# Performance work log

Measured on AMD Instinct MI355X. Metric: run time of the kernel, lower is better.

## Reference

```python
import jax, jax.numpy as jnp
import numpy as np

N = 100000   # nodes
E = 1600000  # edges
IN = 92      # input node feature dim
H = 128      # hidden dim
B = 512      # graphs in batch
GI = 107     # global_info feature dim
L = 5        # conv layers
EPS = 1e-5   # batchnorm eps


def setup_inputs() -> dict:
    key = jax.random.key(0)
    ks = jax.random.split(key, 32)
    s = 0.05
    rn = lambda k, shp: jax.random.normal(k, shp, jnp.float32) * s
    return {
        "x": jax.random.normal(ks[0], (N, IN), jnp.float32),
        "edge_index": jax.random.randint(ks[1], (2, E), 0, N, jnp.int32),
        "edge_dist": jax.random.uniform(ks[2], (E,), jnp.float32),
        "global_info": jax.random.normal(ks[3], (N, GI), jnp.float32),
        "batch": jnp.sort(jax.random.randint(ks[4], (N,), 0, B, jnp.int32)),
        # input projection
        "lin_W": rn(ks[5], (IN, H)), "lin_b": rn(ks[6], (H,)),
        # GCN conv stack
        "conv_W": rn(ks[7], (L, H, H)), "conv_b": rn(ks[8], (L, H)),
        # shared batchnorm affine
        "bn_g": jnp.ones((H,), jnp.float32), "bn_b": jnp.zeros((H,), jnp.float32),
        # global attention
        "gat_in_W": rn(ks[9], (H + GI, H)), "gat_in_b": rn(ks[10], (H,)),
        "gat_lin_W": rn(ks[11], (2, H, H)), "gat_lin_b": rn(ks[12], (2, H)),
        "gat_out_W": rn(ks[13], (H, 1)), "gat_out_b": rn(ks[14], (1,)),
        # Set2Set LSTM (input 2H, hidden H)
        "lstm_Wih": rn(ks[15], (4 * H, 2 * H)), "lstm_Whh": rn(ks[16], (4 * H, H)),
        "lstm_bih": rn(ks[17], (4 * H,)), "lstm_bhh": rn(ks[18], (4 * H,)),
        # MLP head (in_dim = 2H)
        "mlp_W": rn(ks[19], (2 * H, 2 * H)), "mlp_b": rn(ks[20], (2 * H,)),
        "out1_W": rn(ks[21], (2 * H, 32)), "out1_b": rn(ks[22], (32,)),
        "out2_W": rn(ks[23], (32, 1)), "out2_b": rn(ks[24], (1,)),
    }


def _segment_softmax(e, seg, num_seg):
    m = jax.ops.segment_max(e, seg, num_seg)
    ex = jnp.exp(e - m[seg])
    return ex / jax.ops.segment_sum(ex, seg, num_seg)[seg]


def reference(x, edge_index, edge_dist, global_info, batch,
              lin_W, lin_b, conv_W, conv_b, bn_g, bn_b,
              gat_in_W, gat_in_b, gat_lin_W, gat_lin_b, gat_out_W, gat_out_b,
              lstm_Wih, lstm_Whh, lstm_bih, lstm_bhh,
              mlp_W, mlp_b, out1_W, out1_b, out2_W, out2_b):
    src, dst = edge_index[0], edge_index[1]

    x = jax.nn.relu(x @ lin_W + lin_b)

    # GCN normalization (improved=True: self-loop weight 2), identical each layer
    deg = jax.ops.segment_sum(edge_dist, dst, N) + 2.0
    dinv = jax.lax.rsqrt(deg)
    enorm = dinv[src] * edge_dist * dinv[dst]   # [E]
    self_norm = 2.0 * dinv * dinv               # [N]

    prev = x
    for l in range(L):
        xw = x @ conv_W[l]                                                  # [N,H]
        agg = (jax.ops.segment_sum(enorm[:, None] * xw[src], dst, N)
               + self_norm[:, None] * xw + conv_b[l])
        mu = agg.mean(0)
        var = agg.var(0)
        h = bn_g * (agg - mu) * jax.lax.rsqrt(var + EPS) + bn_b             # BN (batch stats)
        x = h + prev                                                         # residual; dropout=identity (eval)
        prev = x

    # global attention -> per-graph softmax node weights
    g = jax.nn.relu(jnp.concatenate([x, global_info], axis=-1) @ gat_in_W + gat_in_b)
    for l in range(2):
        g = jax.nn.relu(g @ gat_lin_W[l] + gat_lin_b[l])
    e = (g @ gat_out_W + gat_out_b)[:, 0]                                    # [N]
    w = _segment_softmax(e, batch, B)
    x = x * w[:, None]

    # Set2Set pooling, 3 processing steps
    hs = jnp.zeros((B, H), x.dtype)
    cs = jnp.zeros((B, H), x.dtype)
    q_star = jnp.zeros((B, 2 * H), x.dtype)
    for _ in range(3):
        gates = q_star @ lstm_Wih.T + hs @ lstm_Whh.T + lstm_bih + lstm_bhh
        i, f, gg, o = jnp.split(gates, 4, axis=-1)
        cs = jax.nn.sigmoid(f) * cs + jax.nn.sigmoid(i) * jnp.tanh(gg)
        hs = jax.nn.sigmoid(o) * jnp.tanh(cs)
        q = hs                                                                # [B,H]
        en = jnp.sum(x * q[batch], axis=-1)                                   # [N]
        a = _segment_softmax(en, batch, B)
        r = jax.ops.segment_sum(a[:, None] * x, batch, B)                      # [B,H]
        q_star = jnp.concatenate([q, r], axis=-1)

    # MLP head
    y = jax.nn.relu(q_star @ mlp_W + mlp_b)
    y = jax.nn.relu(y @ out1_W + out1_b)
    y = y @ out2_W + out2_b
    return y.reshape(1, -1)
```

## Files before the change

kernel.cpp:

```cpp
#include <hip/hip_runtime.h>
#include <math.h>

#define NN 100000
#define NE 1600000
#define DIN 92
#define H 128
#define NB 512
#define DGI 107
#define NL 5

typedef unsigned short u16;
typedef unsigned long long u64;
typedef short bf16x8 __attribute__((ext_vector_type(8)));
typedef float f32x4 __attribute__((ext_vector_type(4)));
typedef _Float16 f16;
typedef _Float16 f16x8 __attribute__((ext_vector_type(8)));
typedef unsigned short u16x8 __attribute__((ext_vector_type(8)));

__device__ __forceinline__ u16 f2bf(float f) {
    unsigned u = __builtin_bit_cast(unsigned, f);
    u += 0x7FFF + ((u >> 16) & 1);
    return (u16)(u >> 16);
}
__device__ __forceinline__ float bf2f(u16 h) {
    unsigned u = ((unsigned)h) << 16;
    return __builtin_bit_cast(float, u);
}

__global__ void __launch_bounds__(128) k_split(const float* __restrict__ src, int Ksrc, int ld_src,
                                               u16* __restrict__ hi, u16* __restrict__ lo,
                                               int ld_dst, int col_off, int Kfill)
{
    int row = blockIdx.x;
    int k = blockIdx.y * 128 + threadIdx.x;
    if (k >= Kfill) return;
    float v = (k < Ksrc) ? src[(size_t)row * ld_src + k] : 0.f;
    u16 h = f2bf(v);
    float r = v - bf2f(h);
    size_t o = (size_t)row * ld_dst + col_off + k;
    hi[o] = h;
    lo[o] = f2bf(r);
}

struct WJobs {
    const float* W[9];
    long long eoff[9];
    int K[9];
    int Kpad[9];
};

__global__ void __launch_bounds__(128) k_splitW_all(WJobs jobs, u16* __restrict__ wthi, u16* __restrict__ wtlo)
{
    int j = blockIdx.z;
    int c = blockIdx.x;
    int k = blockIdx.y * 128 + threadIdx.x;
    int Kp = jobs.Kpad[j];
    if (k >= Kp) return;
    const float* W = jobs.W[j];
    float v = (k < jobs.K[j]) ? W[(size_t)k * H + c] : 0.f;
    u16 h = f2bf(v);
    float r = v - bf2f(h);
    size_t o = (size_t)jobs.eoff[j] + (size_t)c * Kp + k;
    wthi[o] = h;
    wtlo[o] = f2bf(r);
}

#define GBM 128

template<int RELU, int OMODE>
__global__ void __launch_bounds__(256) k_mgemm(
    const u16* __restrict__ A1hi, const u16* __restrict__ A1lo, int lda1, int K1,
    const u16* __restrict__ A2hi, const u16* __restrict__ A2lo, int lda2,
    const u16* __restrict__ Wthi, const u16* __restrict__ Wtlo, int Kpad,
    const float* __restrict__ bias,
    float* __restrict__ Cf, u16* __restrict__ Chi, u16* __restrict__ Clo, int ldsp,
    f16* __restrict__ Ch,
    const float* __restrict__ Gow, const float* __restrict__ GobP, float* __restrict__ Esc,
    int M)
{
    __shared__ __align__(16) u16 As[2][128][40];
    __shared__ __align__(16) u16 Ws[2][128][40];
    int tid = threadIdx.x;
    int w = tid >> 6, l = tid & 63;
    int row0 = blockIdx.x * GBM;
    int lr = l & 15, kq = l >> 4;

    f32x4 acc[2][8];
#pragma unroll
    for (int rf = 0; rf < 2; ++rf)
#pragma unroll
        for (int cf = 0; cf < 8; ++cf)
            acc[rf][cf] = (f32x4){0.f, 0.f, 0.f, 0.f};

    for (int k0 = 0; k0 < Kpad; k0 += 32) {
        const u16* sAh = (k0 < K1) ? A1hi : A2hi;
        const u16* sAl = (k0 < K1) ? A1lo : A2lo;
        int ldc = (k0 < K1) ? lda1 : lda2;
        int kc = (k0 < K1) ? k0 : (k0 - K1);
#pragma unroll
        for (int i = 0; i < 2; ++i) {
            int chunk = tid + i * 256;
            int r = chunk >> 2, q = chunk & 3;
            int gr = row0 + r; if (gr >= M) gr = M - 1;
            int4 va = *(const int4*)(sAh + (size_t)gr * ldc + kc + q * 8);
            int4 vb = *(const int4*)(sAl + (size_t)gr * ldc + kc + q * 8);
            int4 wa = *(const int4*)(Wthi + (size_t)r * Kpad + k0 + q * 8);
            int4 wb = *(const int4*)(Wtlo + (size_t)r * Kpad + k0 + q * 8);
            *(int4*)&As[0][r][q * 8] = va;
            *(int4*)&As[1][r][q * 8] = vb;
            *(int4*)&Ws[0][r][q * 8] = wa;
            *(int4*)&Ws[1][r][q * 8] = wb;
        }
        __syncthreads();

        bf16x8 aH[2], aL[2];
#pragma unroll
        for (int rf = 0; rf < 2; ++rf) {
            aH[rf] = *(const bf16x8*)&As[0][w * 32 + rf * 16 + lr][kq * 8];
            aL[rf] = *(const bf16x8*)&As[1][w * 32 + rf * 16 + lr][kq * 8];
        }
#pragma unroll
        for (int cf = 0; cf < 8; ++cf) {
            bf16x8 bH = *(const bf16x8*)&Ws[0][cf * 16 + lr][kq * 8];
            bf16x8 bL = *(const bf16x8*)&Ws[1][cf * 16 + lr][kq * 8];
#pragma unroll
            for (int rf = 0; rf < 2; ++rf) {
                acc[rf][cf] = __builtin_amdgcn_mfma_f32_16x16x32_bf16(aH[rf], bH, acc[rf][cf], 0, 0, 0);
                acc[rf][cf] = __builtin_amdgcn_mfma_f32_16x16x32_bf16(aH[rf], bL, acc[rf][cf], 0, 0, 0);
                acc[rf][cf] = __builtin_amdgcn_mfma_f32_16x16x32_bf16(aL[rf], bH, acc[rf][cf], 0, 0, 0);
            }
        }
        __syncthreads();
    }

    if (OMODE == 3) {
        float gowv[8], bvv[8];
#pragma unroll
        for (int cf = 0; cf < 8; ++cf) {
            gowv[cf] = Gow[cf * 16 + lr];
            bvv[cf] = bias[cf * 16 + lr];
        }
        float gob0 = GobP[0];
#pragma unroll
        for (int rf = 0; rf < 2; ++rf) {
#pragma unroll
            for (int r = 0; r < 4; ++r) {
                float part = 0.f;
#pragma unroll
                for (int cf = 0; cf < 8; ++cf) {
                    float v = fmaxf(acc[rf][cf][r] + bvv[cf], 0.f);
                    part += v * gowv[cf];
                }
                part += __shfl_xor(part, 1);
                part += __shfl_xor(part, 2);
                part += __shfl_xor(part, 4);
                part += __shfl_xor(part, 8);
                int grow = row0 + w * 32 + rf * 16 + kq * 4 + r;
                if (lr == 0 && grow < M) Esc[grow] = part + gob0;
            }
        }
        return;
    }

#pragma unroll
    for (int cf = 0; cf < 8; ++cf) {
        int col = cf * 16 + lr;
        float bv = bias ? bias[col] : 0.f;
#pragma unroll
        for (int rf = 0; rf < 2; ++rf) {
#pragma unroll
            for (int r = 0; r < 4; ++r) {
                int grow = row0 + w * 32 + rf * 16 + kq * 4 + r;
                if (grow < M) {
                    float v = acc[rf][cf][r] + bv;
                    if (RELU) v = fmaxf(v, 0.f);
                    if (OMODE == 0) Cf[(size_t)grow * H + col] = v;
                    if (OMODE == 1) {
                        u16 hh = f2bf(v);
                        Chi[(size_t)grow * ldsp + col] = hh;
                        Clo[(size_t)grow * ldsp + col] = f2bf(v - bf2f(hh));
                    }
                    if (OMODE == 2) Ch[(size_t)grow * H + col] = (f16)v;
                }
            }
        }
    }
}

__global__ void __launch_bounds__(256) k_deg2(const int* __restrict__ dst, const float* __restrict__ ed,
                                              u64* __restrict__ degcnt, int* __restrict__ rank)
{
    int e = blockIdx.x * 256 + threadIdx.x;
    if (e < NE) {
        int d = dst[e];
        u64 pk = ((u64)1 << 40) | (u64)(ed[e] * 16777216.0f);
        u64 old = atomicAdd(&degcnt[d], pk);
        rank[e] = (int)(old >> 40);
    }
}

__global__ void __launch_bounds__(256) k_dinv2(const u64* __restrict__ degcnt,
                                               float* __restrict__ dinv, float* __restrict__ selfn,
                                               int* __restrict__ cnt)
{
    int n = blockIdx.x * 256 + threadIdx.x;
    if (n < NN) {
        u64 v = degcnt[n];
        int c = (int)(v >> 40);
        float deg = (float)((double)(v & (((u64)1 << 40) - 1)) * (1.0 / 16777216.0));
        float d = deg + 2.0f;
        float dv = 1.0f / sqrtf(d);
        dinv[n] = dv;
        selfn[n] = 2.0f * dv * dv;
        cnt[n] = c;
    }
}

__global__ void __launch_bounds__(256) k_blocksum(const int* __restrict__ cnt, int* __restrict__ bsum, int n)
{
    __shared__ int red[256];
    int t = threadIdx.x;
    int base = blockIdx.x * 1024;
    int s = 0;
#pragma unroll
    for (int j = 0; j < 4; ++j) {
        int i = base + j * 256 + t;
        if (i < n) s += cnt[i];
    }
    red[t] = s; __syncthreads();
    for (int off = 128; off; off >>= 1) {
        if (t < off) red[t] += red[t + off];
        __syncthreads();
    }
    if (t == 0) bsum[blockIdx.x] = red[0];
}

__global__ void k_scanbsum(const int* __restrict__ bsum, int* __restrict__ boff, int nb,
                           int* __restrict__ rp_last, int total)
{
    if (threadIdx.x == 0 && blockIdx.x == 0) {
        int s = 0;
        for (int i = 0; i < nb; ++i) { boff[i] = s; s += bsum[i]; }
        rp_last[0] = total;
    }
}

__global__ void __launch_bounds__(1024) k_scanchunk(const int* __restrict__ cnt, const int* __restrict__ boff,
                                                    int* __restrict__ rp, int n)
{
    __shared__ int sc[1024];
    int t = threadIdx.x;
    int i = blockIdx.x * 1024 + t;
    int own = (i < n) ? cnt[i] : 0;
    sc[t] = own;
    __syncthreads();
    for (int off = 1; off < 1024; off <<= 1) {
        int v = (t >= off) ? sc[t - off] : 0;
        __syncthreads();
        sc[t] += v;
        __syncthreads();
    }
    if (i < n) rp[i] = boff[blockIdx.x] + sc[t] - own;
}

__global__ void __launch_bounds__(256) k_place2(const int* __restrict__ src, const int* __restrict__ dst,
                                                const float* __restrict__ ed, const float* __restrict__ dinv,
                                                const int* __restrict__ rp, const int* __restrict__ rank,
                                                int2* __restrict__ ew)
{
    int e = blockIdx.x * 256 + threadIdx.x;
    if (e < NE) {
        int d = dst[e], s = src[e];
        int pos = rp[d] + rank[e];
        float w = dinv[s] * ed[e] * dinv[d];
        ew[pos] = make_int2(s, __builtin_bit_cast(int, w));
    }
}

__global__ void __launch_bounds__(256) k_spmm(
    const f16* __restrict__ xwh, const int* __restrict__ rp,
    const int2* __restrict__ ew,
    const float* __restrict__ selfn, const float* __restrict__ cb,
    f16* __restrict__ aggh, double* __restrict__ stats)
{
    int tid = threadIdx.x;
    int slot = tid >> 4;
    int sl = tid & 15;
    int f0 = sl * 8;
    float cbv[8], psum[8], psq[8];
#pragma unroll
    for (int j = 0; j < 8; ++j) { cbv[j] = cb[f0 + j]; psum[j] = 0.f; psq[j] = 0.f; }
    int base = blockIdx.x * 32 + slot * 2;

    for (int i = 0; i < 2; ++i) {
        int n = base + i;
        if (n >= NN) break;
        f16x8 xv = *(const f16x8*)(xwh + (size_t)n * H + f0);
        float sn = selfn[n];
        float a0[8], a1[8], a2[8], a3[8];
#pragma unroll
        for (int j = 0; j < 8; ++j) {
            a0[j] = sn * (float)xv[j] + cbv[j];
            a1[j] = 0.f; a2[j] = 0.f; a3[j] = 0.f;
        }
        int e = rp[n], end = rp[n + 1];
        for (; e + 4 <= end; e += 4) {
            int2 p0 = ew[e], p1 = ew[e + 1], p2 = ew[e + 2], p3 = ew[e + 3];
            float w0 = __builtin_bit_cast(float, p0.y);
            float w1 = __builtin_bit_cast(float, p1.y);
            float w2 = __builtin_bit_cast(float, p2.y);
            float w3 = __builtin_bit_cast(float, p3.y);
            f16x8 v0 = *(const f16x8*)(xwh + (size_t)p0.x * H + f0);
            f16x8 v1 = *(const f16x8*)(xwh + (size_t)p1.x * H + f0);
            f16x8 v2 = *(const f16x8*)(xwh + (size_t)p2.x * H + f0);
            f16x8 v3 = *(const f16x8*)(xwh + (size_t)p3.x * H + f0);
#pragma unroll
            for (int j = 0; j < 8; ++j) {
                a0[j] += w0 * (float)v0[j];
                a1[j] += w1 * (float)v1[j];
                a2[j] += w2 * (float)v2[j];
                a3[j] += w3 * (float)v3[j];
            }
        }
        for (; e < end; ++e) {
            int2 p = ew[e];
            float w0 = __builtin_bit_cast(float, p.y);
            f16x8 v0 = *(const f16x8*)(xwh + (size_t)p.x * H + f0);
#pragma unroll
            for (int j = 0; j < 8; ++j) a0[j] += w0 * (float)v0[j];
        }
        float ax[8];
        f16x8 ah;
#pragma unroll
        for (int j = 0; j < 8; ++j) {
            ax[j] = (a0[j] + a1[j]) + (a2[j] + a3[j]);
            psum[j] += ax[j];
            psq[j] += ax[j] * ax[j];
            ah[j] = (f16)ax[j];
        }
        *(f16x8*)(aggh + (size_t)n * H + f0) = ah;
    }

    __shared__ float ssum[16][128], ssq[16][128];
#pragma unroll
    for (int j = 0; j < 8; ++j) { ssum[slot][f0 + j] = psum[j]; ssq[slot][f0 + j] = psq[j]; }
    __syncthreads();
    if (tid < 128) {
        float s = 0.f, q = 0.f;
#pragma unroll
        for (int j = 0; j < 16; ++j) { s += ssum[j][tid]; q += ssq[j][tid]; }
        atomicAdd(&stats[tid], (double)s);
        atomicAdd(&stats[128 + tid], (double)q);
    }
}

__global__ void k_finalize(double* __restrict__ stats, const float* __restrict__ bn_g,
                           const float* __restrict__ bn_b, float* __restrict__ scale,
                           float* __restrict__ shift)
{
    int f = threadIdx.x;
    double mu = stats[f] / (double)NN;
    double var = stats[128 + f] / (double)NN - mu * mu;
    double rs = 1.0 / sqrt(var + 1e-5);
    float sc = (float)((double)bn_g[f] * rs);
    scale[f] = sc;
    shift[f] = (float)((double)bn_b[f] - mu * (double)sc);
    stats[f] = 0.0;
    stats[128 + f] = 0.0;
}

__global__ void __launch_bounds__(256) k_bnres(const f16* __restrict__ aggh, const float* __restrict__ scale,
                                               const float* __restrict__ shift,
                                               u16* __restrict__ xhi, u16* __restrict__ xlo)
{
    int i8 = blockIdx.x * 256 + threadIdx.x;
    if (i8 >= NN * 16) return;
    int f0 = (i8 & 15) * 8;
    f16x8 a = ((const f16x8*)aggh)[i8];
    u16x8 hh = ((const u16x8*)xhi)[i8];
    u16x8 ll = ((const u16x8*)xlo)[i8];
#pragma unroll
    for (int j = 0; j < 8; ++j) {
        float v = bf2f(hh[j]) + bf2f(ll[j]) + (float)a[j] * scale[f0 + j] + shift[f0 + j];
        u16 h = f2bf(v);
        hh[j] = h;
        ll[j] = f2bf(v - bf2f(h));
    }
    ((u16x8*)xhi)[i8] = hh;
    ((u16x8*)xlo)[i8] = ll;
}

__global__ void __launch_bounds__(256) k_gcnt(const int* __restrict__ batch, int* __restrict__ gcnt)
{
    int n = blockIdx.x * 256 + threadIdx.x;
    if (n < NN) atomicAdd(&gcnt[batch[n]], 1);
}

__global__ void __launch_bounds__(512) k_goff(const int* __restrict__ gcnt, int* __restrict__ goff)
{
    __shared__ int sc[512];
    int t = threadIdx.x;
    sc[t] = gcnt[t];
    __syncthreads();
    for (int off = 1; off < 512; off <<= 1) {
        int v = (t >= off) ? sc[t - off] : 0;
        __syncthreads();
        sc[t] += v;
        __syncthreads();
    }
    goff[t + 1] = sc[t];
    if (t == 0) goff[0] = 0;
}

__global__ void __launch_bounds__(256) k_segsoftmax(const float* __restrict__ e, const int* __restrict__ goff,
                                                    float* __restrict__ w)
{
    int b = blockIdx.x;
    int beg = goff[b], end = goff[b + 1];
    int t = threadIdx.x;
    __shared__ float red[8], red2[8];
    float m = -INFINITY;
    for (int i = beg + t; i < end; i += 256) m = fmaxf(m, e[i]);
    for (int off = 32; off; off >>= 1) m = fmaxf(m, __shfl_down(m, off));
    if ((t & 63) == 0) red[t >> 6] = m;
    __syncthreads();
    float m0 = fmaxf(fmaxf(red[0], red[1]), fmaxf(red[2], red[3]));
    float s = 0.f;
    for (int i = beg + t; i < end; i += 256) s += expf(e[i] - m0);
    for (int off = 32; off; off >>= 1) s += __shfl_down(s, off);
    if ((t & 63) == 0) red2[t >> 6] = s;
    __syncthreads();
    float s0 = red2[0] + red2[1] + red2[2] + red2[3];
    for (int i = beg + t; i < end; i += 256) w[i] = expf(e[i] - m0) / s0;
}

__global__ void __launch_bounds__(256) k_scalex(const u16* __restrict__ xhi, const u16* __restrict__ xlo,
                                                const float* __restrict__ w, float* __restrict__ xf)
{
    int i4 = blockIdx.x * 256 + threadIdx.x;
    if (i4 >= NN * 32) return;
    float ww = w[i4 >> 5];
    ushort4 hh = ((const ushort4*)xhi)[i4];
    ushort4 ll = ((const ushort4*)xlo)[i4];
    float4 v;
    v.x = (bf2f(hh.x) + bf2f(ll.x)) * ww;
    v.y = (bf2f(hh.y) + bf2f(ll.y)) * ww;
    v.z = (bf2f(hh.z) + bf2f(ll.z)) * ww;
    v.w = (bf2f(hh.w) + bf2f(ll.w)) * ww;
    ((float4*)xf)[i4] = v;
}

__device__ __forceinline__ float sigmoidf_(float v) { return 1.f / (1.f + expf(-v)); }

__global__ void __launch_bounds__(256) k_gateslstm(
    const float* __restrict__ qstar, const float* __restrict__ Wih, const float* __restrict__ Whh,
    const float* __restrict__ bih, const float* __restrict__ bhh,
    float* __restrict__ cs, float* __restrict__ hs)
{
    __shared__ float qs[8][256];
    __shared__ float hh[8][128];
    __shared__ float gs[8][512];
    int t = threadIdx.x;
    int b0 = blockIdx.x * 8;
    for (int i = t; i < 8 * 256; i += 256) qs[i >> 8][i & 255] = qstar[b0 * 256 + i];
    for (int i = t; i < 8 * 128; i += 256) hh[i >> 7][i & 127] = hs[b0 * 128 + i];
    __syncthreads();
    for (int gg = t; gg < 512; gg += 256) {
        float acc[8];
        float bb = bih[gg] + bhh[gg];
#pragma unroll
        for (int g = 0; g < 8; ++g) acc[g] = bb;
        const float4* w4 = (const float4*)(Wih + (size_t)gg * 256);
        for (int k = 0; k < 64; ++k) {
            float4 w = w4[k];
#pragma unroll
            for (int g = 0; g < 8; ++g) {
                float4 q = *(const float4*)&qs[g][k * 4];
                acc[g] += q.x * w.x + q.y * w.y + q.z * w.z + q.w * w.w;
            }
        }
        const float4* v4 = (const float4*)(Whh + (size_t)gg * 128);
        for (int k = 0; k < 32; ++k) {
            float4 w = v4[k];
#pragma unroll
            for (int g = 0; g < 8; ++g) {
                float4 q = *(const float4*)&hh[g][k * 4];
                acc[g] += q.x * w.x + q.y * w.y + q.z * w.z + q.w * w.w;
            }
        }
#pragma unroll
        for (int g = 0; g < 8; ++g) gs[g][gg] = acc[g];
    }
    __syncthreads();
    for (int i = t; i < 1024; i += 256) {
        int g = i >> 7, f = i & 127;
        int idx = (b0 + g) * 128 + f;
        float gi = gs[g][f], gf = gs[g][128 + f], gg2 = gs[g][256 + f], go = gs[g][384 + f];
        float c = sigmoidf_(gf) * cs[idx] + sigmoidf_(gi) * tanhf(gg2);
        cs[idx] = c;
        hs[idx] = sigmoidf_(go) * tanhf(c);
    }
}

__global__ void __launch_bounds__(256) k_en(const float* __restrict__ x, const float* __restrict__ hs,
                                            const int* __restrict__ batch, float* __restrict__ en)
{
    int wave = threadIdx.x >> 6, lane = threadIdx.x & 63;
    int n = blockIdx.x * 4 + wave;
    if (n >= NN) return;
    int b = batch[n];
    float2 xv = *(const float2*)(x + (size_t)n * H + lane * 2);
    float2 qv = *(const float2*)(hs + (size_t)b * H + lane * 2);
    float p = xv.x * qv.x + xv.y * qv.y;
    for (int off = 32; off; off >>= 1) p += __shfl_down(p, off);
    if (lane == 0) en[n] = p;
}

__global__ void __launch_bounds__(128) k_r(const float* __restrict__ a, const float* __restrict__ x,
                                           const int* __restrict__ goff, const float* __restrict__ hs,
                                           float* __restrict__ qstar)
{
    int b = blockIdx.x, f = threadIdx.x;
    int beg = goff[b], end = goff[b + 1];
    float acc = 0.f;
    for (int i = beg; i < end; ++i) acc += a[i] * x[(size_t)i * H + f];
    qstar[b * 256 + f] = hs[b * 128 + f];
    qstar[b * 256 + 128 + f] = acc;
}

__global__ void __launch_bounds__(256) k_head1(const float* __restrict__ qstar, const float* __restrict__ W,
                                               const float* __restrict__ bias, float* __restrict__ y1)
{
    __shared__ float qs[256];
    int b = blockIdx.x, t = threadIdx.x;
    qs[t] = qstar[b * 256 + t];
    __syncthreads();
    float acc = bias[t];
    for (int k = 0; k < 256; ++k) acc += qs[k] * W[k * 256 + t];
    y1[b * 256 + t] = fmaxf(acc, 0.f);
}

__global__ void __launch_bounds__(256) k_head2(const float* __restrict__ y1, const float* __restrict__ W1,
                                               const float* __restrict__ b1, const float* __restrict__ W2,
                                               const float* __restrict__ b2, float* __restrict__ out)
{
    __shared__ float ys[256];
    __shared__ float z[32];
    int b = blockIdx.x, t = threadIdx.x;
    ys[t] = y1[b * 256 + t];
    __syncthreads();
    if (t < 32) {
        float acc = b1[t];
        for (int k = 0; k < 256; ++k) acc += ys[k] * W1[k * 32 + t];
        z[t] = fmaxf(acc, 0.f);
    }
    __syncthreads();
    if (t == 0) {
        float s = b2[0];
        for (int j = 0; j < 32; ++j) s += z[j] * W2[j];
        out[b] = s;
    }
}

extern "C" void kernel_launch(void* const* d_in, const int* in_sizes, int n_in,
                              void* d_out, int out_size, void* d_ws, size_t ws_size,
                              hipStream_t stream)
{
    const float* in_x        = (const float*)d_in[0];
    const int*   edge_index  = (const int*)d_in[1];
    const float* edge_dist   = (const float*)d_in[2];
    const float* global_info = (const float*)d_in[3];
    const int*   batch       = (const int*)d_in[4];
    const float* lin_W  = (const float*)d_in[5];
    const float* lin_b  = (const float*)d_in[6];
    const float* conv_W = (const float*)d_in[7];
    const float* conv_b = (const float*)d_in[8];
    const float* bn_g   = (const float*)d_in[9];
    const float* bn_b   = (const float*)d_in[10];
    const float* gat_in_W  = (const float*)d_in[11];
    const float* gat_in_b  = (const float*)d_in[12];
    const float* gat_lin_W = (const float*)d_in[13];
    const float* gat_lin_b = (const float*)d_in[14];
    const float* gat_out_W = (const float*)d_in[15];
    const float* gat_out_b = (const float*)d_in[16];
    const float* lstm_Wih = (const float*)d_in[17];
    const float* lstm_Whh = (const float*)d_in[18];
    const float* lstm_bih = (const float*)d_in[19];
    const float* lstm_bhh = (const float*)d_in[20];
    const float* mlp_W  = (const float*)d_in[21];
    const float* mlp_b  = (const float*)d_in[22];
    const float* out1_W = (const float*)d_in[23];
    const float* out1_b = (const float*)d_in[24];
    const float* out2_W = (const float*)d_in[25];
    const float* out2_b = (const float*)d_in[26];
    float* out = (float*)d_out;

    const int* e_src = edge_index;
    const int* e_dst = edge_index + NE;

    char* p = (char*)d_ws;
    auto alloc = [&](size_t bytes) -> void* {
        void* r = (void*)p;
        p += (bytes + 255) & ~(size_t)255;
        return r;
    };
    u16*    cx_hi = (u16*)alloc((size_t)NN * H * 2);
    u16*    cx_lo = (u16*)alloc((size_t)NN * H * 2);
    float*  xw    = (float*)alloc((size_t)NN * H * 4);
    float*  agg   = (float*)alloc((size_t)NN * H * 4);
    u16*    wthi  = (u16*)alloc((size_t)160000 * 2);
    u16*    wtlo  = (u16*)alloc((size_t)160000 * 2);
    float*  dinv  = (float*)alloc((size_t)NN * 4);
    float*  selfn = (float*)alloc((size_t)NN * 4);
    int*    cnt   = (int*)alloc((size_t)NN * 4);
    int*    rp    = (int*)alloc((size_t)(NN + 1) * 4);
    int*    bsum  = (int*)alloc(128 * 4);
    int*    boff  = (int*)alloc(128 * 4);
    int2*   ew    = (int2*)alloc((size_t)NE * 8);
    double* stats = (double*)alloc(256 * 8);
    float*  scale = (float*)alloc(128 * 4);
    float*  shift = (float*)alloc(128 * 4);

    f16*   xwh    = (f16*)xw;
    f16*   aggh   = (f16*)agg;
    u64*   degcnt = (u64*)agg;
    int*   rank   = (int*)((char*)agg + (1 << 20));
    u16*   gi_hi  = (u16*)agg;
    u16*   gi_lo  = gi_hi + (size_t)NN * H;
    float* esc    = dinv;
    float* wn     = selfn;
    int*   gcnt   = cnt;
    int*   goff   = cnt + NB;
    float* hs     = (float*)ew;
    float* csb    = hs + NB * H;
    float* qstar  = csb + NB * H;
    float* gates  = qstar + NB * 2 * H;
    float* y1     = gates + NB * 4 * H;

    const int GB_E = (NE + 255) / 256;
    const int GB_N = (NN + 255) / 256;
    const int NCH = (NN + 1023) / 1024;
    const int GB_MG = (NN + GBM - 1) / GBM;
    const int GB_SPMM = (NN + 31) / 32;
    const int GB_V4 = (NN * 32) / 256;
    const int GB_V8 = (NN * 16) / 256 + 1;
    const int GB_W = (NN + 3) / 4;

    WJobs jobs;
    const float* Wl[9] = {lin_W, conv_W, conv_W + (size_t)H * H, conv_W + (size_t)2 * H * H,
                          conv_W + (size_t)3 * H * H, conv_W + (size_t)4 * H * H,
                          gat_in_W, gat_lin_W, gat_lin_W + (size_t)H * H};
    int Ks[9]  = {DIN, H, H, H, H, H, H + DGI, H, H};
    int Kps[9] = {96, H, H, H, H, H, 256, H, H};
    long long eoffs[9];
    long long eo = 0;
    for (int i = 0; i < 9; ++i) {
        jobs.W[i] = Wl[i]; jobs.K[i] = Ks[i]; jobs.Kpad[i] = Kps[i]; jobs.eoff[i] = eo;
        eoffs[i] = eo;
        eo += (long long)128 * Kps[i];
    }
    k_splitW_all<<<dim3(128, 2, 9), 128, 0, stream>>>(jobs, wthi, wtlo);

    hipMemsetAsync(degcnt, 0, (size_t)NN * 8, stream);
    hipMemsetAsync(stats, 0, 256 * 8, stream);
    k_deg2<<<GB_E, 256, 0, stream>>>(e_dst, edge_dist, degcnt, rank);
    k_dinv2<<<GB_N, 256, 0, stream>>>(degcnt, dinv, selfn, cnt);
    k_blocksum<<<NCH, 256, 0, stream>>>(cnt, bsum, NN);
    k_scanbsum<<<1, 64, 0, stream>>>(bsum, boff, NCH, rp + NN, NE);
    k_scanchunk<<<NCH, 1024, 0, stream>>>(cnt, boff, rp, NN);
    k_place2<<<GB_E, 256, 0, stream>>>(e_src, e_dst, edge_dist, dinv, rp, rank, ew);

    k_split<<<dim3(NN, 1), 128, 0, stream>>>(in_x, DIN, DIN, cx_hi, cx_lo, H, 0, 96);
    k_mgemm<1, 1><<<GB_MG, 256, 0, stream>>>(cx_hi, cx_lo, H, 96, cx_hi, cx_lo, H,
                                             wthi + eoffs[0], wtlo + eoffs[0], 96, lin_b,
                                             nullptr, cx_hi, cx_lo, H, nullptr,
                                             nullptr, nullptr, nullptr, NN);

    for (int l = 0; l < NL; ++l) {
        k_mgemm<0, 2><<<GB_MG, 256, 0, stream>>>(cx_hi, cx_lo, H, H, cx_hi, cx_lo, H,
                                                 wthi + eoffs[1 + l], wtlo + eoffs[1 + l], H, nullptr,
                                                 nullptr, nullptr, nullptr, 0, xwh,
                                                 nullptr, nullptr, nullptr, NN);
        k_spmm<<<GB_SPMM, 256, 0, stream>>>(xwh, rp, ew, selfn, conv_b + (size_t)l * H, aggh, stats);
        k_finalize<<<1, 128, 0, stream>>>(stats, bn_g, bn_b, scale, shift);
        k_bnres<<<GB_V8, 256, 0, stream>>>(aggh, scale, shift, cx_hi, cx_lo);
    }

    k_split<<<dim3(NN, 1), 128, 0, stream>>>(global_info, DGI, DGI, gi_hi, gi_lo, H, 0, H);
    k_mgemm<1, 1><<<GB_MG, 256, 0, stream>>>(cx_hi, cx_lo, H, H, gi_hi, gi_lo, H,
                                             wthi + eoffs[6], wtlo + eoffs[6], 256, gat_in_b,
                                             nullptr, gi_hi, gi_lo, H, nullptr,
                                             nullptr, nullptr, nullptr, NN);
    k_mgemm<1, 1><<<GB_MG, 256, 0, stream>>>(gi_hi, gi_lo, H, H, gi_hi, gi_lo, H,
                                             wthi + eoffs[7], wtlo + eoffs[7], H, gat_lin_b,
                                             nullptr, gi_hi, gi_lo, H, nullptr,
                                             nullptr, nullptr, nullptr, NN);
    k_mgemm<1, 3><<<GB_MG, 256, 0, stream>>>(gi_hi, gi_lo, H, H, gi_hi, gi_lo, H,
                                             wthi + eoffs[8], wtlo + eoffs[8], H, gat_lin_b + H,
                                             nullptr, nullptr, nullptr, 0, nullptr,
                                             gat_out_W, gat_out_b, esc, NN);
    hipMemsetAsync(gcnt, 0, NB * 4, stream);
    k_gcnt<<<GB_N, 256, 0, stream>>>(batch, gcnt);
    k_goff<<<1, 512, 0, stream>>>(gcnt, goff);
    k_segsoftmax<<<NB, 256, 0, stream>>>(esc, goff, wn);
    k_scalex<<<GB_V4, 256, 0, stream>>>(cx_hi, cx_lo, wn, xw);

    hipMemsetAsync(hs, 0, (size_t)NB * H * 4, stream);
    hipMemsetAsync(csb, 0, (size_t)NB * H * 4, stream);
    hipMemsetAsync(qstar, 0, (size_t)NB * 2 * H * 4, stream);
    for (int it = 0; it < 3; ++it) {
        k_gateslstm<<<NB / 8, 256, 0, stream>>>(qstar, lstm_Wih, lstm_Whh, lstm_bih, lstm_bhh, csb, hs);
        k_en<<<GB_W, 256, 0, stream>>>(xw, hs, batch, esc);
        k_segsoftmax<<<NB, 256, 0, stream>>>(esc, goff, wn);
        k_r<<<NB, 128, 0, stream>>>(wn, xw, goff, hs, qstar);
    }

    k_head1<<<NB, 256, 0, stream>>>(qstar, mlp_W, mlp_b, y1);
    k_head2<<<NB, 256, 0, stream>>>(y1, out1_W, out1_b, out2_W, out2_b, out);
}
```

Baseline: 1.679 ms.

## Pack CSR edges into 32 bits, fuse Set2Set steps, compute graph offsets directly

Edge entries are packed into one 32-bit word holding a 17-bit source index and an fp16 weight, which halves the edge-list traffic in each SpMM layer. Those loads and the aggregate stores now use nontemporal hints. The Set2Set attention (dot product, segment softmax, weighted sum) is fused into one kernel per graph instead of three launches. Graph offsets are computed from the sorted batch array by boundary detection instead of atomic counting plus a scan. Storing edge weights in fp16 loses precision, and the packing limits node indices to 17 bits.

After: 1.547 ms. 7.9% less time.

```diff
diff --git a/kernel.cpp b/kernel.cpp
--- a/kernel.cpp
+++ b/kernel.cpp
@@ -10,6 +10,7 @@
 #define NL 5
 
 typedef unsigned short u16;
+typedef unsigned int u32;
 typedef unsigned long long u64;
 typedef short bf16x8 __attribute__((ext_vector_type(8)));
 typedef float f32x4 __attribute__((ext_vector_type(4)));
@@ -266,20 +267,22 @@
 __global__ void __launch_bounds__(256) k_place2(const int* __restrict__ src, const int* __restrict__ dst,
                                                 const float* __restrict__ ed, const float* __restrict__ dinv,
                                                 const int* __restrict__ rp, const int* __restrict__ rank,
-                                                int2* __restrict__ ew)
+                                                u32* __restrict__ ew)
 {
     int e = blockIdx.x * 256 + threadIdx.x;
     if (e < NE) {
         int d = dst[e], s = src[e];
         int pos = rp[d] + rank[e];
         float w = dinv[s] * ed[e] * dinv[d];
-        ew[pos] = make_int2(s, __builtin_bit_cast(int, w));
+        f16 wh = (f16)w;
+        u32 wb = (u32)__builtin_bit_cast(u16, wh);
+        ew[pos] = (wb << 17) | (u32)s;
     }
 }
 
 __global__ void __launch_bounds__(256) k_spmm(
     const f16* __restrict__ xwh, const int* __restrict__ rp,
-    const int2* __restrict__ ew,
+    const u32* __restrict__ ew,
     const float* __restrict__ selfn, const float* __restrict__ cb,
     f16* __restrict__ aggh, double* __restrict__ stats)
 {
@@ -305,15 +308,18 @@
         }
         int e = rp[n], end = rp[n + 1];
         for (; e + 4 <= end; e += 4) {
-            int2 p0 = ew[e], p1 = ew[e + 1], p2 = ew[e + 2], p3 = ew[e + 3];
-            float w0 = __builtin_bit_cast(float, p0.y);
-            float w1 = __builtin_bit_cast(float, p1.y);
-            float w2 = __builtin_bit_cast(float, p2.y);
-            float w3 = __builtin_bit_cast(float, p3.y);
-            f16x8 v0 = *(const f16x8*)(xwh + (size_t)p0.x * H + f0);
-            f16x8 v1 = *(const f16x8*)(xwh + (size_t)p1.x * H + f0);
-            f16x8 v2 = *(const f16x8*)(xwh + (size_t)p2.x * H + f0);
-            f16x8 v3 = *(const f16x8*)(xwh + (size_t)p3.x * H + f0);
+            u32 p0 = __builtin_nontemporal_load(ew + e);
+            u32 p1 = __builtin_nontemporal_load(ew + e + 1);
+            u32 p2 = __builtin_nontemporal_load(ew + e + 2);
+            u32 p3 = __builtin_nontemporal_load(ew + e + 3);
+            float w0 = (float)__builtin_bit_cast(f16, (u16)(p0 >> 17));
+            float w1 = (float)__builtin_bit_cast(f16, (u16)(p1 >> 17));
+            float w2 = (float)__builtin_bit_cast(f16, (u16)(p2 >> 17));
+            float w3 = (float)__builtin_bit_cast(f16, (u16)(p3 >> 17));
+            f16x8 v0 = *(const f16x8*)(xwh + (size_t)(p0 & 0x1FFFF) * H + f0);
+            f16x8 v1 = *(const f16x8*)(xwh + (size_t)(p1 & 0x1FFFF) * H + f0);
+            f16x8 v2 = *(const f16x8*)(xwh + (size_t)(p2 & 0x1FFFF) * H + f0);
+            f16x8 v3 = *(const f16x8*)(xwh + (size_t)(p3 & 0x1FFFF) * H + f0);
 #pragma unroll
             for (int j = 0; j < 8; ++j) {
                 a0[j] += w0 * (float)v0[j];
@@ -323,9 +329,9 @@
             }
         }
         for (; e < end; ++e) {
-            int2 p = ew[e];
-            float w0 = __builtin_bit_cast(float, p.y);
-            f16x8 v0 = *(const f16x8*)(xwh + (size_t)p.x * H + f0);
+            u32 p = __builtin_nontemporal_load(ew + e);
+            float w0 = (float)__builtin_bit_cast(f16, (u16)(p >> 17));
+            f16x8 v0 = *(const f16x8*)(xwh + (size_t)(p & 0x1FFFF) * H + f0);
 #pragma unroll
             for (int j = 0; j < 8; ++j) a0[j] += w0 * (float)v0[j];
         }
@@ -338,7 +344,7 @@
             psq[j] += ax[j] * ax[j];
             ah[j] = (f16)ax[j];
         }
-        *(f16x8*)(aggh + (size_t)n * H + f0) = ah;
+        __builtin_nontemporal_store(ah, (f16x8*)(aggh + (size_t)n * H + f0));
     }
 
     __shared__ float ssum[16][128], ssq[16][128];
@@ -390,26 +396,16 @@
     ((u16x8*)xlo)[i8] = ll;
 }
 
-__global__ void __launch_bounds__(256) k_gcnt(const int* __restrict__ batch, int* __restrict__ gcnt)
+__global__ void __launch_bounds__(256) k_goff2(const int* __restrict__ batch, int* __restrict__ goff)
 {
     int n = blockIdx.x * 256 + threadIdx.x;
-    if (n < NN) atomicAdd(&gcnt[batch[n]], 1);
-}
-
-__global__ void __launch_bounds__(512) k_goff(const int* __restrict__ gcnt, int* __restrict__ goff)
-{
-    __shared__ int sc[512];
-    int t = threadIdx.x;
-    sc[t] = gcnt[t];
-    __syncthreads();
-    for (int off = 1; off < 512; off <<= 1) {
-        int v = (t >= off) ? sc[t - off] : 0;
-        __syncthreads();
-        sc[t] += v;
-        __syncthreads();
-    }
-    goff[t + 1] = sc[t];
-    if (t == 0) goff[0] = 0;
+    if (n >= NN) return;
+    int b = batch[n];
+    if (n == 0) {
+        for (int j = 0; j <= b; ++j) goff[j] = 0;
+    }
+    int nb = (n == NN - 1) ? NB : batch[n + 1];
+    for (int j = b + 1; j <= nb; ++j) goff[j] = n + 1;
 }
 
 __global__ void __launch_bounds__(256) k_segsoftmax(const float* __restrict__ e, const int* __restrict__ goff,
@@ -502,30 +498,54 @@
     }
 }
 
-__global__ void __launch_bounds__(256) k_en(const float* __restrict__ x, const float* __restrict__ hs,
-                                            const int* __restrict__ batch, float* __restrict__ en)
-{
-    int wave = threadIdx.x >> 6, lane = threadIdx.x & 63;
-    int n = blockIdx.x * 4 + wave;
-    if (n >= NN) return;
-    int b = batch[n];
-    float2 xv = *(const float2*)(x + (size_t)n * H + lane * 2);
-    float2 qv = *(const float2*)(hs + (size_t)b * H + lane * 2);
-    float p = xv.x * qv.x + xv.y * qv.y;
-    for (int off = 32; off; off >>= 1) p += __shfl_down(p, off);
-    if (lane == 0) en[n] = p;
-}
-
-__global__ void __launch_bounds__(128) k_r(const float* __restrict__ a, const float* __restrict__ x,
-                                           const int* __restrict__ goff, const float* __restrict__ hs,
-                                           float* __restrict__ qstar)
-{
-    int b = blockIdx.x, f = threadIdx.x;
+__global__ void __launch_bounds__(256) k_s2s(const float* __restrict__ x, const float* __restrict__ hs,
+                                             const int* __restrict__ goff,
+                                             float* __restrict__ esc, float* __restrict__ qstar)
+{
+    __shared__ float q[128];
+    __shared__ float red[4], red2[4];
+    __shared__ float partr[128];
+    int b = blockIdx.x, t = threadIdx.x;
     int beg = goff[b], end = goff[b + 1];
+    if (t < 128) q[t] = hs[b * 128 + t];
+    __syncthreads();
+
+    int wv = t >> 6, ln = t & 63;
+    float m = -INFINITY;
+    for (int i = beg + wv; i < end; i += 4) {
+        float2 xv = *(const float2*)(x + (size_t)i * H + ln * 2);
+        float2 qv = *(const float2*)(q + ln * 2);
+        float pd = xv.x * qv.x + xv.y * qv.y;
+        for (int off = 32; off; off >>= 1) pd += __shfl_down(pd, off);
+        pd = __shfl(pd, 0);
+        if (ln == 0) esc[i] = pd;
+        m = fmaxf(m, pd);
+    }
+    if (ln == 0) red[wv] = m;
+    __syncthreads();
+    float m0 = fmaxf(fmaxf(red[0], red[1]), fmaxf(red[2], red[3]));
+    float s = 0.f;
+    for (int i = beg + t; i < end; i += 256) {
+        float e = expf(esc[i] - m0);
+        esc[i] = e;
+        s += e;
+    }
+    for (int off = 32; off; off >>= 1) s += __shfl_down(s, off);
+    if (ln == 0) red2[wv] = s;
+    __syncthreads();
+    float s0 = red2[0] + red2[1] + red2[2] + red2[3];
+    float inv = (s0 > 0.f) ? 1.f / s0 : 0.f;
+    int f = t & 127, half = t >> 7;
     float acc = 0.f;
-    for (int i = beg; i < end; ++i) acc += a[i] * x[(size_t)i * H + f];
-    qstar[b * 256 + f] = hs[b * 128 + f];
-    qstar[b * 256 + 128 + f] = acc;
+    for (int i = beg + half; i < end; i += 2)
+        acc += esc[i] * x[(size_t)i * H + f];
+    if (half) partr[f] = acc;
+    __syncthreads();
+    if (!half) {
+        acc += partr[f];
+        qstar[b * 256 + f] = q[f];
+        qstar[b * 256 + 128 + f] = acc * inv;
+    }
 }
 
 __global__ void __launch_bounds__(256) k_head1(const float* __restrict__ qstar, const float* __restrict__ W,
@@ -616,7 +636,7 @@
     int*    rp    = (int*)alloc((size_t)(NN + 1) * 4);
     int*    bsum  = (int*)alloc(128 * 4);
     int*    boff  = (int*)alloc(128 * 4);
-    int2*   ew    = (int2*)alloc((size_t)NE * 8);
+    u32*    ew    = (u32*)alloc((size_t)NE * 4);
     double* stats = (double*)alloc(256 * 8);
     float*  scale = (float*)alloc(128 * 4);
     float*  shift = (float*)alloc(128 * 4);
@@ -629,13 +649,11 @@
     u16*   gi_lo  = gi_hi + (size_t)NN * H;
     float* esc    = dinv;
     float* wn     = selfn;
-    int*   gcnt   = cnt;
-    int*   goff   = cnt + NB;
+    int*   goff   = cnt;
     float* hs     = (float*)ew;
     float* csb    = hs + NB * H;
     float* qstar  = csb + NB * H;
-    float* gates  = qstar + NB * 2 * H;
-    float* y1     = gates + NB * 4 * H;
+    float* y1     = qstar + NB * 2 * H;
 
     const int GB_E = (NE + 255) / 256;
     const int GB_N = (NN + 255) / 256;
@@ -644,7 +662,6 @@
     const int GB_SPMM = (NN + 31) / 32;
     const int GB_V4 = (NN * 32) / 256;
     const int GB_V8 = (NN * 16) / 256 + 1;
-    const int GB_W = (NN + 3) / 4;
 
     WJobs jobs;
     const float* Wl[9] = {lin_W, conv_W, conv_W + (size_t)H * H, conv_W + (size_t)2 * H * H,
@@ -699,9 +716,7 @@
                                              wthi + eoffs[8], wtlo + eoffs[8], H, gat_lin_b + H,
                                              nullptr, nullptr, nullptr, 0, nullptr,
                                              gat_out_W, gat_out_b, esc, NN);
-    hipMemsetAsync(gcnt, 0, NB * 4, stream);
-    k_gcnt<<<GB_N, 256, 0, stream>>>(batch, gcnt);
-    k_goff<<<1, 512, 0, stream>>>(gcnt, goff);
+    k_goff2<<<GB_N, 256, 0, stream>>>(batch, goff);
     k_segsoftmax<<<NB, 256, 0, stream>>>(esc, goff, wn);
     k_scalex<<<GB_V4, 256, 0, stream>>>(cx_hi, cx_lo, wn, xw);
 
@@ -710,9 +725,7 @@
     hipMemsetAsync(qstar, 0, (size_t)NB * 2 * H * 4, stream);
     for (int it = 0; it < 3; ++it) {
         k_gateslstm<<<NB / 8, 256, 0, stream>>>(qstar, lstm_Wih, lstm_Whh, lstm_bih, lstm_bhh, csb, hs);
-        k_en<<<GB_W, 256, 0, stream>>>(xw, hs, batch, esc);
-        k_segsoftmax<<<NB, 256, 0, stream>>>(esc, goff, wn);
-        k_r<<<NB, 128, 0, stream>>>(wn, xw, goff, hs, qstar);
+        k_s2s<<<NB, 256, 0, stream>>>(xw, hs, goff, esc, qstar);
     }
 
     k_head1<<<NB, 256, 0, stream>>>(qstar, mlp_W, mlp_b, y1);
```
